# Performance work log

Measured on AMD Instinct MI355X. Metric: run time of the kernel, lower is better.

The kernel has to match this reference:

```python
import jax, jax.numpy as jnp
import numpy as np

EMBED = 1024
HEADS = 16
HEAD_DIM = EMBED // HEADS
N, S = 4, 2048


def setup_inputs() -> dict:
    key = jax.random.key(0)
    ks = jax.random.split(key, 8)
    inp = {
        "queries": jax.random.normal(ks[0], (N, S, EMBED), jnp.float32),
        "keys": jax.random.normal(ks[1], (N, S, EMBED), jnp.float32),
        "values": jax.random.normal(ks[2], (N, S, EMBED), jnp.float32),
        # torch Linear weights stored as [out, in]
        "Wq": jax.random.normal(ks[3], (HEAD_DIM, HEAD_DIM), jnp.float32) / np.sqrt(HEAD_DIM),
        "Wk": jax.random.normal(ks[4], (HEAD_DIM, HEAD_DIM), jnp.float32) / np.sqrt(HEAD_DIM),
        "Wv": jax.random.normal(ks[5], (HEAD_DIM, HEAD_DIM), jnp.float32) / np.sqrt(HEAD_DIM),
        "Wo": jax.random.normal(ks[6], (EMBED, EMBED), jnp.float32) / np.sqrt(EMBED),
        "bo": jax.random.normal(ks[7], (EMBED,), jnp.float32) * 0.01,
    }
    return inp


def reference(queries, keys, values, Wq, Wk, Wv, Wo, bo):
    n, qlen, _ = queries.shape
    klen = keys.shape[1]
    # split heads: [N, L, H, D]
    q = queries.reshape(n, qlen, HEADS, HEAD_DIM)
    k = keys.reshape(n, klen, HEADS, HEAD_DIM)
    v = values.reshape(n, klen, HEADS, HEAD_DIM)
    # per-head linear projections (torch Linear: x @ W.T)
    q = jnp.einsum('nqhd,ed->nqhe', q, Wq)
    k = jnp.einsum('nkhd,ed->nkhe', k, Wk)
    v = jnp.einsum('nkhd,ed->nkhe', v, Wv)
    # attention scores [N, H, Q, K]; NOTE: scaled by sqrt(embed_size) as in original
    energy = jnp.einsum('nqhd,nkhd->nhqk', q, k)
    attn = jax.nn.softmax(energy / jnp.sqrt(jnp.float32(EMBED)), axis=3)
    out = jnp.einsum('nhqk,nkhd->nqhd', attn, v).reshape(n, qlen, EMBED)
    return out @ Wo.T + bo
```

## Files before the change

### kernel.cpp

```cpp
#include <hip/hip_runtime.h>

#define HEADS 16
#define HD 64
#define EMB 1024
#define NB 4
#define SEQ 2048

typedef __attribute__((ext_vector_type(8))) short bf16x8;
typedef __attribute__((ext_vector_type(4))) float f32x4;
typedef unsigned short ushort_t;

__device__ __forceinline__ unsigned short f2bf(float f) {
  union { float f; unsigned u; } v; v.f = f;
  unsigned r = v.u + 0x7FFFu + ((v.u >> 16) & 1u);
  return (unsigned short)(r >> 16);
}

__device__ __forceinline__ unsigned pk2bf(float a, float b) {
  unsigned r;
  asm("v_cvt_pk_bf16_f32 %0, %1, %2" : "=v"(r) : "v"(a), "v"(b));
  return r;
}

__device__ __forceinline__ bf16x8 pk8(float4 a, float4 b) {
  union { bf16x8 v; unsigned u[4]; } r;
  r.u[0] = pk2bf(a.x, a.y);
  r.u[1] = pk2bf(a.z, a.w);
  r.u[2] = pk2bf(b.x, b.y);
  r.u[3] = pk2bf(b.z, b.w);
  return r.v;
}

__device__ __forceinline__ void gload_lds16(const void* g, void* l) {
  __builtin_amdgcn_global_load_lds((const __attribute__((address_space(1))) void*)g,
                                   (__attribute__((address_space(3))) void*)l,
                                   16, 0, 0);
}

__device__ __forceinline__ f32x4 mfma16(bf16x8 a, bf16x8 b, f32x4 c) {
  return __builtin_amdgcn_mfma_f32_16x16x32_bf16(a, b, c, 0, 0, 0);
}

__global__ __launch_bounds__(256) void cvt_wo(const float* __restrict__ Wo,
                                              ushort_t* __restrict__ Wo16) {
  int idx = (blockIdx.x * 256 + threadIdx.x) * 4;
  float4 v = *(const float4*)(Wo + idx);
  uint2 u;
  u.x = pk2bf(v.x, v.y);
  u.y = pk2bf(v.z, v.w);
  *(uint2*)(Wo16 + idx) = u;
}

__global__ __launch_bounds__(256) void proj_kernel(
    const float* __restrict__ xq, const float* __restrict__ xk, const float* __restrict__ xv,
    const float* __restrict__ Wq, const float* __restrict__ Wk, const float* __restrict__ Wv,
    ushort_t* __restrict__ Qp, ushort_t* __restrict__ Kp, ushort_t* __restrict__ VpT) {
  int bid = blockIdx.x;
  int tensor = bid >> 9;
  int rem = bid & 511;
  int nh = rem >> 3;
  int st = rem & 7;
  int n = nh >> 4, h = nh & 15;
  int tid = threadIdx.x;
  int w = tid >> 6, l = tid & 63;
  int i = l & 15, g = l >> 4;
  int s0 = st * 256 + w * 64;

  const float* X = (tensor == 0) ? xq : (tensor == 1) ? xk : xv;
  const float* W = (tensor == 0) ? Wq : (tensor == 1) ? Wk : Wv;
  float wscale = (tensor == 0) ? 0.045084220027780106f : 1.0f;

  bf16x8 bfrag[4][2];
#pragma unroll
  for (int nt = 0; nt < 4; ++nt)
#pragma unroll
    for (int ks = 0; ks < 2; ++ks) {
      const float* wp = W + (i + 16 * nt) * 64 + 32 * ks + 8 * g;
      float4 w0 = *(const float4*)wp;
      float4 w1 = *(const float4*)(wp + 4);
      w0.x *= wscale; w0.y *= wscale; w0.z *= wscale; w0.w *= wscale;
      w1.x *= wscale; w1.y *= wscale; w1.z *= wscale; w1.w *= wscale;
      bfrag[nt][ks] = pk8(w0, w1);
    }

  f32x4 acc[4][4];
  const f32x4 z4 = {0.f, 0.f, 0.f, 0.f};
#pragma unroll
  for (int a = 0; a < 4; ++a)
#pragma unroll
    for (int b = 0; b < 4; ++b) acc[a][b] = z4;

  const float* Xb = X + (long)n * SEQ * EMB + h * HD;
#pragma unroll
  for (int ks = 0; ks < 2; ++ks) {
#pragma unroll
    for (int mt = 0; mt < 4; ++mt) {
      const float* xp = Xb + (long)(s0 + 16 * mt + i) * EMB + 32 * ks + 8 * g;
      float4 x0 = *(const float4*)xp;
      float4 x1 = *(const float4*)(xp + 4);
      bf16x8 a = pk8(x0, x1);
#pragma unroll
      for (int nt = 0; nt < 4; ++nt)
        acc[mt][nt] = mfma16(a, bfrag[nt][ks], acc[mt][nt]);
    }
  }

  if (tensor < 2) {
    ushort_t* O = ((tensor == 0) ? Qp : Kp) + (long)nh * SEQ * HD;
#pragma unroll
    for (int mt = 0; mt < 4; ++mt)
#pragma unroll
      for (int nt = 0; nt < 4; ++nt)
#pragma unroll
        for (int r = 0; r < 4; ++r)
          O[(long)(s0 + 16 * mt + 4 * g + r) * HD + i + 16 * nt] = f2bf(acc[mt][nt][r]);
  } else {
    ushort_t* O = VpT + (long)nh * HD * SEQ;
#pragma unroll
    for (int mt = 0; mt < 4; ++mt)
#pragma unroll
      for (int nt = 0; nt < 4; ++nt) {
        uint2 u;
        u.x = pk2bf(acc[mt][nt][0], acc[mt][nt][1]);
        u.y = pk2bf(acc[mt][nt][2], acc[mt][nt][3]);
        *(uint2*)&O[(long)(i + 16 * nt) * SEQ + s0 + 16 * mt + 4 * g] = u;
      }
  }
}

__global__ __launch_bounds__(256) void attn_kernel(
    const ushort_t* __restrict__ Qp, const ushort_t* __restrict__ Kp,
    const ushort_t* __restrict__ VpT, ushort_t* __restrict__ AO) {
  __shared__ ushort_t lds[32768];
  ushort_t* Klds = lds;
  ushort_t* Vlds = lds + 8192;
  ushort_t* Plds = lds + 16384;

  int bid = blockIdx.x;
  int xcd = bid & 7, idx = bid >> 3;
  int nh = xcd * 8 + (idx >> 3), qb = idx & 7;
  int tid = threadIdx.x, w = tid >> 6, l = tid & 63, i = l & 15, g = l >> 4;
  int q0 = qb * 256 + w * 64;

  const ushort_t* Qb = Qp + (long)nh * SEQ * HD;
  const ushort_t* Kb = Kp + (long)nh * SEQ * HD;
  const ushort_t* Vb = VpT + (long)nh * HD * SEQ;

  bf16x8 qf[4][2];
#pragma unroll
  for (int qt = 0; qt < 4; ++qt)
#pragma unroll
    for (int ks = 0; ks < 2; ++ks)
      qf[qt][ks] = *(const bf16x8*)(Qb + (long)(q0 + 16 * qt + i) * HD + 32 * ks + 8 * g);

  f32x4 o[4][4];
  const f32x4 z4 = {0.f, 0.f, 0.f, 0.f};
#pragma unroll
  for (int a = 0; a < 4; ++a)
#pragma unroll
    for (int b = 0; b < 4; ++b) o[a][b] = z4;
  float lrun[4];
#pragma unroll
  for (int qt = 0; qt < 4; ++qt) lrun[qt] = 0.f;

  auto stage = [&](int buf, int kv0) {
    const ushort_t* kb = Kb + (long)kv0 * HD;
    const ushort_t* vb = Vb + kv0;
    ushort_t* lk = Klds + buf * 4096;
    ushort_t* lv = Vlds + buf * 4096;
#pragma unroll
    for (int rep = 0; rep < 2; ++rep) {
      int p = tid + 256 * rep;
      int row = p >> 3, c = p & 7;
      int sc = ((c ^ (row & 7)) * 8);
      gload_lds16(kb + row * HD + sc, lk + p * 8);
      gload_lds16(vb + (long)row * SEQ + sc, lv + p * 8);
    }
  };

  stage(0, 0);
  asm volatile("s_waitcnt vmcnt(0)" ::: "memory");
  __syncthreads();

  for (int it = 0; it < 32; ++it) {
    int cur = it & 1;
    if (it < 31) stage(cur ^ 1, (it + 1) * 64);
    const ushort_t* lk = Klds + cur * 4096;
    const ushort_t* lv = Vlds + cur * 4096;
    ushort_t* pl = Plds + w * 4096;

    f32x4 s[4][4];
#pragma unroll
    for (int a = 0; a < 4; ++a)
#pragma unroll
      for (int b = 0; b < 4; ++b) s[a][b] = z4;
#pragma unroll
    for (int ks = 0; ks < 2; ++ks)
#pragma unroll
      for (int mt = 0; mt < 4; ++mt) {
        int row = i + 16 * mt;
        bf16x8 a = *(const bf16x8*)((const char*)lk + row * 128 +
                                    (((4 * ks + g) ^ (row & 7)) << 4));
#pragma unroll
        for (int qt = 0; qt < 4; ++qt)
          s[mt][qt] = mfma16(a, qf[qt][ks], s[mt][qt]);
      }

#pragma unroll
    for (int qt = 0; qt < 4; ++qt) {
      float psum = 0.f;
      int q = i + 16 * qt;
#pragma unroll
      for (int mt = 0; mt < 4; ++mt) {
        float p0, p1, p2, p3;
        asm("v_exp_f32 %0, %4\n\t"
            "v_exp_f32 %1, %5\n\t"
            "v_exp_f32 %2, %6\n\t"
            "v_exp_f32 %3, %7"
            : "=&v"(p0), "=&v"(p1), "=&v"(p2), "=&v"(p3)
            : "v"(s[mt][qt][0]), "v"(s[mt][qt][1]),
              "v"(s[mt][qt][2]), "v"(s[mt][qt][3]));
        psum += (p0 + p1) + (p2 + p3);
        uint2 u;
        u.x = pk2bf(p0, p1);
        u.y = pk2bf(p2, p3);
        *(uint2*)((char*)pl + q * 128 + ((32 * mt + 8 * g) ^ ((q & 7) << 4))) = u;
      }
      lrun[qt] += psum;
    }

#pragma unroll
    for (int ks = 0; ks < 2; ++ks) {
      bf16x8 pf[4];
#pragma unroll
      for (int qt = 0; qt < 4; ++qt) {
        int q = i + 16 * qt;
        pf[qt] = *(const bf16x8*)((const char*)pl + q * 128 +
                                  (((4 * ks + g) ^ (q & 7)) << 4));
      }
#pragma unroll
      for (int mtd = 0; mtd < 4; ++mtd) {
        int row = i + 16 * mtd;
        bf16x8 a = *(const bf16x8*)((const char*)lv + row * 128 +
                                    (((4 * ks + g) ^ (row & 7)) << 4));
#pragma unroll
        for (int qt = 0; qt < 4; ++qt)
          o[mtd][qt] = mfma16(a, pf[qt], o[mtd][qt]);
      }
    }

    asm volatile("s_waitcnt vmcnt(0)" ::: "memory");
    __syncthreads();
  }

#pragma unroll
  for (int qt = 0; qt < 4; ++qt) {
    float lt = lrun[qt];
    lt += __shfl_xor(lt, 16);
    lt += __shfl_xor(lt, 32);
    float linv = 1.0f / lt;
    int q = i + 16 * qt;
#pragma unroll
    for (int mtd = 0; mtd < 4; ++mtd) {
      uint2 u;
      u.x = pk2bf(o[mtd][qt][0] * linv, o[mtd][qt][1] * linv);
      u.y = pk2bf(o[mtd][qt][2] * linv, o[mtd][qt][3] * linv);
      *(uint2*)((char*)(Plds + w * 4096) + q * 128 +
                ((32 * mtd + 8 * g) ^ ((q & 7) << 4))) = u;
    }
  }
  __syncthreads();
  int n = nh >> 4, h = nh & 15;
  ushort_t* aob = AO + ((long)n * SEQ + q0) * EMB + h * HD;
#pragma unroll
  for (int rep = 0; rep < 8; ++rep) {
    int qr = (l >> 3) + 8 * rep;
    int c = l & 7;
    bf16x8 v = *(const bf16x8*)((const char*)(Plds + w * 4096) + qr * 128 +
                                ((c ^ (qr & 7)) << 4));
    *(bf16x8*)(aob + (long)qr * EMB + 8 * c) = v;
  }
}

__global__ __launch_bounds__(256) void ogemm_kernel(
    const ushort_t* __restrict__ A, const ushort_t* __restrict__ B16,
    const float* __restrict__ bo, float* __restrict__ out) {
  __shared__ ushort_t lds[16384];
  ushort_t* Al = lds;
  ushort_t* Bl = lds + 8192;
  int bid = blockIdx.x;
  int xcd = bid & 7, idx = bid >> 3;
  int m0 = (xcd * 8 + (idx >> 3)) * 128, n0 = (idx & 7) * 128;
  int tid = threadIdx.x, w = tid >> 6, l = tid & 63, i = l & 15, g = l >> 4;
  int wr = w >> 1, wc = w & 1;

  auto stage = [&](int buf, int k0) {
#pragma unroll
    for (int rep = 0; rep < 2; ++rep) {
      int p = tid + 256 * rep;
      int row = p >> 2, c = p & 3;
      gload_lds16(A + (long)(m0 + row) * EMB + k0 + 8 * c, Al + buf * 4096 + p * 8);
      gload_lds16(B16 + (long)(n0 + row) * EMB + k0 + 8 * c, Bl + buf * 4096 + p * 8);
    }
  };

  f32x4 acc[4][4];
  const f32x4 z4 = {0.f, 0.f, 0.f, 0.f};
#pragma unroll
  for (int a = 0; a < 4; ++a)
#pragma unroll
    for (int b = 0; b < 4; ++b) acc[a][b] = z4;

  stage(0, 0);
  asm volatile("s_waitcnt vmcnt(0)" ::: "memory");
  __syncthreads();
  for (int kt = 0; kt < 32; ++kt) {
    int cur = kt & 1;
    if (kt < 31) stage(cur ^ 1, (kt + 1) * 32);
    const ushort_t* al = Al + cur * 4096;
    const ushort_t* bl = Bl + cur * 4096;
    bf16x8 af[4], bfr[4];
#pragma unroll
    for (int mt = 0; mt < 4; ++mt)
      af[mt] = *(const bf16x8*)((const char*)al + (wr * 64 + 16 * mt + i) * 64 + g * 16);
#pragma unroll
    for (int nt = 0; nt < 4; ++nt)
      bfr[nt] = *(const bf16x8*)((const char*)bl + (wc * 64 + 16 * nt + i) * 64 + g * 16);
#pragma unroll
    for (int mt = 0; mt < 4; ++mt)
#pragma unroll
      for (int nt = 0; nt < 4; ++nt)
        acc[mt][nt] = mfma16(af[mt], bfr[nt], acc[mt][nt]);
    asm volatile("s_waitcnt vmcnt(0)" ::: "memory");
    __syncthreads();
  }
#pragma unroll
  for (int nt = 0; nt < 4; ++nt) {
    int col = n0 + wc * 64 + 16 * nt + i;
    float bv = bo[col];
#pragma unroll
    for (int mt = 0; mt < 4; ++mt)
#pragma unroll
      for (int r = 0; r < 4; ++r)
        out[(long)(m0 + wr * 64 + 16 * mt + 4 * g + r) * EMB + col] = acc[mt][nt][r] + bv;
  }
}

extern "C" void kernel_launch(void* const* d_in, const int* in_sizes, int n_in,
                              void* d_out, int out_size, void* d_ws, size_t ws_size,
                              hipStream_t stream) {
  const float* q  = (const float*)d_in[0];
  const float* k  = (const float*)d_in[1];
  const float* v  = (const float*)d_in[2];
  const float* Wq = (const float*)d_in[3];
  const float* Wk = (const float*)d_in[4];
  const float* Wv = (const float*)d_in[5];
  const float* Wo = (const float*)d_in[6];
  const float* bo = (const float*)d_in[7];
  float* out = (float*)d_out;
  char* ws = (char*)d_ws;
  ushort_t* Qp   = (ushort_t*)(ws);
  ushort_t* Kp   = (ushort_t*)(ws + 16777216L);
  ushort_t* VpT  = (ushort_t*)(ws + 2 * 16777216L);
  ushort_t* AO   = (ushort_t*)(ws + 3 * 16777216L);
  ushort_t* Wo16 = (ushort_t*)(ws + 4 * 16777216L);

  cvt_wo<<<dim3(1024), dim3(256), 0, stream>>>(Wo, Wo16);
  proj_kernel<<<dim3(1536), dim3(256), 0, stream>>>(q, k, v, Wq, Wk, Wv, Qp, Kp, VpT);
  attn_kernel<<<dim3(512), dim3(256), 0, stream>>>(Qp, Kp, VpT, AO);
  ogemm_kernel<<<dim3(512), dim3(256), 0, stream>>>(AO, Wo16, bo, out);
}
```

Measured before the change: 150.3 us.

## Load K/V tiles directly into registers instead of shared LDS double buffer

Each wave now reads its K and V MFMA operand fragments straight from global memory into registers, prefetching the next tile's K after the softmax and the next V after the PV product. This removes the LDS K/V staging buffers and the per-iteration block barriers, and halves LDS usage, which may raise occupancy. In exchange, all four waves of a block redundantly fetch the same K/V tiles from global memory/L2, and load latency is hidden only by in-register prefetching. The register footprint also grows.

```diff
diff --git a/kernel.cpp b/kernel.cpp
--- a/kernel.cpp
+++ b/kernel.cpp
@@ -131,10 +131,7 @@
 __global__ __launch_bounds__(256) void attn_kernel(
     const ushort_t* __restrict__ Qp, const ushort_t* __restrict__ Kp,
     const ushort_t* __restrict__ VpT, ushort_t* __restrict__ AO) {
-  __shared__ ushort_t lds[32768];
-  ushort_t* Klds = lds;
-  ushort_t* Vlds = lds + 8192;
-  ushort_t* Plds = lds + 16384;
+  __shared__ ushort_t lds[16384];
 
   int bid = blockIdx.x;
   int xcd = bid & 7, idx = bid >> 3;
@@ -163,31 +160,19 @@
 #pragma unroll
   for (int qt = 0; qt < 4; ++qt) lrun[qt] = 0.f;
 
-  auto stage = [&](int buf, int kv0) {
-    const ushort_t* kb = Kb + (long)kv0 * HD;
-    const ushort_t* vb = Vb + kv0;
-    ushort_t* lk = Klds + buf * 4096;
-    ushort_t* lv = Vlds + buf * 4096;
-#pragma unroll
-    for (int rep = 0; rep < 2; ++rep) {
-      int p = tid + 256 * rep;
-      int row = p >> 3, c = p & 7;
-      int sc = ((c ^ (row & 7)) * 8);
-      gload_lds16(kb + row * HD + sc, lk + p * 8);
-      gload_lds16(vb + (long)row * SEQ + sc, lv + p * 8);
-    }
-  };
-
-  stage(0, 0);
-  asm volatile("s_waitcnt vmcnt(0)" ::: "memory");
-  __syncthreads();
+  bf16x8 kf[4][2], vf[4][2];
+#pragma unroll
+  for (int mt = 0; mt < 4; ++mt)
+#pragma unroll
+    for (int ks = 0; ks < 2; ++ks) {
+      kf[mt][ks] = *(const bf16x8*)(Kb + (long)(16 * mt + i) * HD + 32 * ks + 8 * g);
+      vf[mt][ks] = *(const bf16x8*)(Vb + (long)(i + 16 * mt) * SEQ + 32 * ks + 8 * g);
+    }
+
+  ushort_t* pl0 = lds + w * 4096;
 
   for (int it = 0; it < 32; ++it) {
-    int cur = it & 1;
-    if (it < 31) stage(cur ^ 1, (it + 1) * 64);
-    const ushort_t* lk = Klds + cur * 4096;
-    const ushort_t* lv = Vlds + cur * 4096;
-    ushort_t* pl = Plds + w * 4096;
+    char* pl = (char*)pl0;
 
     f32x4 s[4][4];
 #pragma unroll
@@ -197,14 +182,10 @@
 #pragma unroll
     for (int ks = 0; ks < 2; ++ks)
 #pragma unroll
-      for (int mt = 0; mt < 4; ++mt) {
-        int row = i + 16 * mt;
-        bf16x8 a = *(const bf16x8*)((const char*)lk + row * 128 +
-                                    (((4 * ks + g) ^ (row & 7)) << 4));
+      for (int mt = 0; mt < 4; ++mt)
 #pragma unroll
         for (int qt = 0; qt < 4; ++qt)
-          s[mt][qt] = mfma16(a, qf[qt][ks], s[mt][qt]);
-      }
+          s[mt][qt] = mfma16(kf[mt][ks], qf[qt][ks], s[mt][qt]);
 
 #pragma unroll
     for (int qt = 0; qt < 4; ++qt) {
@@ -224,33 +205,43 @@
         uint2 u;
         u.x = pk2bf(p0, p1);
         u.y = pk2bf(p2, p3);
-        *(uint2*)((char*)pl + q * 128 + ((32 * mt + 8 * g) ^ ((q & 7) << 4))) = u;
+        *(uint2*)(pl + q * 128 + ((32 * mt + 8 * g) ^ ((q & 7) << 4))) = u;
       }
       lrun[qt] += psum;
     }
 
+    if (it < 31) {
+      const ushort_t* kn = Kb + (long)(it + 1) * 64 * HD;
+#pragma unroll
+      for (int mt = 0; mt < 4; ++mt)
+#pragma unroll
+        for (int ks = 0; ks < 2; ++ks)
+          kf[mt][ks] = *(const bf16x8*)(kn + (long)(16 * mt + i) * HD + 32 * ks + 8 * g);
+    }
+
 #pragma unroll
     for (int ks = 0; ks < 2; ++ks) {
       bf16x8 pf[4];
 #pragma unroll
       for (int qt = 0; qt < 4; ++qt) {
         int q = i + 16 * qt;
-        pf[qt] = *(const bf16x8*)((const char*)pl + q * 128 +
-                                  (((4 * ks + g) ^ (q & 7)) << 4));
+        pf[qt] = *(const bf16x8*)(pl + q * 128 + (((4 * ks + g) ^ (q & 7)) << 4));
       }
 #pragma unroll
-      for (int mtd = 0; mtd < 4; ++mtd) {
-        int row = i + 16 * mtd;
-        bf16x8 a = *(const bf16x8*)((const char*)lv + row * 128 +
-                                    (((4 * ks + g) ^ (row & 7)) << 4));
+      for (int mtd = 0; mtd < 4; ++mtd)
 #pragma unroll
         for (int qt = 0; qt < 4; ++qt)
-          o[mtd][qt] = mfma16(a, pf[qt], o[mtd][qt]);
-      }
-    }
-
-    asm volatile("s_waitcnt vmcnt(0)" ::: "memory");
-    __syncthreads();
+          o[mtd][qt] = mfma16(vf[mtd][ks], pf[qt], o[mtd][qt]);
+    }
+
+    if (it < 31) {
+      const ushort_t* vn = Vb + (it + 1) * 64;
+#pragma unroll
+      for (int mtd = 0; mtd < 4; ++mtd)
+#pragma unroll
+        for (int ks = 0; ks < 2; ++ks)
+          vf[mtd][ks] = *(const bf16x8*)(vn + (long)(i + 16 * mtd) * SEQ + 32 * ks + 8 * g);
+    }
   }
 
 #pragma unroll
@@ -265,19 +256,16 @@
       uint2 u;
       u.x = pk2bf(o[mtd][qt][0] * linv, o[mtd][qt][1] * linv);
       u.y = pk2bf(o[mtd][qt][2] * linv, o[mtd][qt][3] * linv);
-      *(uint2*)((char*)(Plds + w * 4096) + q * 128 +
-                ((32 * mtd + 8 * g) ^ ((q & 7) << 4))) = u;
-    }
-  }
-  __syncthreads();
+      *(uint2*)((char*)pl0 + q * 128 + ((32 * mtd + 8 * g) ^ ((q & 7) << 4))) = u;
+    }
+  }
   int n = nh >> 4, h = nh & 15;
   ushort_t* aob = AO + ((long)n * SEQ + q0) * EMB + h * HD;
 #pragma unroll
   for (int rep = 0; rep < 8; ++rep) {
     int qr = (l >> 3) + 8 * rep;
     int c = l & 7;
-    bf16x8 v = *(const bf16x8*)((const char*)(Plds + w * 4096) + qr * 128 +
-                                ((c ^ (qr & 7)) << 4));
+    bf16x8 v = *(const bf16x8*)((const char*)pl0 + qr * 128 + ((c ^ (qr & 7)) << 4));
     *(bf16x8*)(aob + (long)qr * EMB + 8 * c) = v;
   }
 }
```

Result: slower. 190.0 us (+26.4%).
